# Kernel tuning notes

Hardware: AMD Instinct MI355X
Metric: run time of the kernel (lower is better)

## Reference

```python
import jax, jax.numpy as jnp
import numpy as np

B, S, D, H, FF = 4, 2048, 1024, 16, 4096
HD = D // H
EPS = 1e-5


def layer_norm(x, g, b):
    mu = jnp.mean(x, axis=-1, keepdims=True)
    var = jnp.mean(jnp.square(x - mu), axis=-1, keepdims=True)
    return (x - mu) * jax.lax.rsqrt(var + EPS) * g + b


def setup_inputs() -> dict:
    key = jax.random.key(0)
    ks = jax.random.split(key, 8)
    s_d = 1.0 / np.sqrt(D)
    s_ff = 1.0 / np.sqrt(FF)
    return {
        "x": jax.random.normal(ks[0], (B, S, D), dtype=jnp.float32),
        "Wq": jax.random.normal(ks[1], (D, D), dtype=jnp.float32) * s_d,
        "bq": jnp.zeros((D,), jnp.float32),
        "Wk": jax.random.normal(ks[2], (D, D), dtype=jnp.float32) * s_d,
        "bk": jnp.zeros((D,), jnp.float32),
        "Wv": jax.random.normal(ks[3], (D, D), dtype=jnp.float32) * s_d,
        "bv": jnp.zeros((D,), jnp.float32),
        "g1": jnp.ones((D,), jnp.float32),
        "beta1": jnp.zeros((D,), jnp.float32),
        "g2": jnp.ones((D,), jnp.float32),
        "beta2": jnp.zeros((D,), jnp.float32),
        "W1": jax.random.normal(ks[4], (D, FF), dtype=jnp.float32) * s_d,
        "b1": jnp.zeros((FF,), jnp.float32),
        "W2": jax.random.normal(ks[5], (FF, D), dtype=jnp.float32) * s_ff,
        "b2": jnp.zeros((D,), jnp.float32),
    }


def reference(x, Wq, bq, Wk, bk, Wv, bv, g1, beta1, g2, beta2, W1, b1, W2, b2):
    # pre-LN attention (self.layer_norm in the original)
    h = layer_norm(x, g1, beta1)
    q = (h @ Wq + bq).reshape(B, S, H, HD)
    k = (h @ Wk + bk).reshape(B, S, H, HD)
    v = (h @ Wv + bv).reshape(B, S, H, HD)
    scores = jnp.einsum("bqhd,bkhd->bhqk", q, k) / np.sqrt(HD)
    probs = jax.nn.softmax(scores, axis=-1)
    attn = jnp.einsum("bhqk,bkhd->bqhd", probs, v).reshape(B, S, D)
    y = attn + x
    # second LN (self.LN), then FFN; note original adds residual from LN output
    f = layer_norm(y, g2, beta2)
    ff = jnp.maximum(f @ W1 + b1, 0.0) @ W2 + b2
    return f + ff
```

## Files before the change

### kernel.cpp

```cpp
#include <hip/hip_runtime.h>
#include <hip/hip_bf16.h>
#include <cstdint>
#include <cstddef>

#define B_   4
#define S_   2048
#define D_   1024
#define H_   16
#define HD_  64
#define FF_  4096
#define MTOT (B_*S_)

typedef __bf16 bf16;
typedef bf16  bf16x8 __attribute__((ext_vector_type(8)));
typedef bf16  bf16x4 __attribute__((ext_vector_type(4)));
typedef float f32x4  __attribute__((ext_vector_type(4)));

#define LOG2E 1.44269504088896340736f

__device__ __forceinline__ void async16(const bf16* g, bf16* l) {
  __builtin_amdgcn_global_load_lds(
      (const __attribute__((address_space(1))) unsigned int*)g,
      (__attribute__((address_space(3))) unsigned int*)l,
      16, 0, 0);
}

__global__ void wcast_t(const float* __restrict__ W, bf16* __restrict__ Wt,
                        int K, int N) {
  __shared__ float t[32][33];
  const int k0 = blockIdx.y * 32, n0 = blockIdx.x * 32;
  const int tx = threadIdx.x, ty = threadIdx.y;
#pragma unroll
  for (int r = ty; r < 32; r += 8)
    t[r][tx] = W[(size_t)(k0 + r) * N + n0 + tx];
  __syncthreads();
#pragma unroll
  for (int r = ty; r < 32; r += 8)
    Wt[(size_t)(n0 + r) * K + k0 + tx] = (bf16)t[tx][r];
}

__global__ void ln_fused(const float* __restrict__ xin, const float* __restrict__ res,
                         const float* __restrict__ gamma, const float* __restrict__ beta,
                         bf16* __restrict__ out) {
  const int row = blockIdx.x, tid = threadIdx.x;
  const int lane = tid & 63, w = tid >> 6;
  f32x4 v = *(const f32x4*)(xin + (size_t)row * D_ + tid * 4);
  if (res) {
    f32x4 r = *(const f32x4*)(res + (size_t)row * D_ + tid * 4);
    v += r;
  }
  float sum = v[0] + v[1] + v[2] + v[3];
  float sq  = v[0]*v[0] + v[1]*v[1] + v[2]*v[2] + v[3]*v[3];
#pragma unroll
  for (int d = 1; d < 64; d <<= 1) {
    sum += __shfl_xor(sum, d);
    sq  += __shfl_xor(sq, d);
  }
  __shared__ float red[8];
  if (lane == 0) { red[w] = sum; red[4 + w] = sq; }
  __syncthreads();
  sum = red[0] + red[1] + red[2] + red[3];
  sq  = red[4] + red[5] + red[6] + red[7];
  const float mu   = sum * (1.f / D_);
  const float rstd = rsqrtf(sq * (1.f / D_) - mu * mu + 1e-5f);
  f32x4 g  = *(const f32x4*)(gamma + tid * 4);
  f32x4 bt = *(const f32x4*)(beta  + tid * 4);
  bf16x4 ov;
#pragma unroll
  for (int j = 0; j < 4; j++)
    ov[j] = (bf16)((v[j] - mu) * rstd * g[j] + bt[j]);
  *(bf16x4*)(out + (size_t)row * D_ + tid * 4) = ov;
}

template <int EPI>
__global__ void gemm_bt(const bf16* __restrict__ A, const bf16* __restrict__ Bt,
                        const float* __restrict__ bias, void* __restrict__ Cout,
                        const bf16* __restrict__ addf, int M, int N, int K) {
  __shared__ bf16 As[128 * 32];
  __shared__ bf16 Bs[128 * 32];
  const int tid = threadIdx.x;
  const int lane = tid & 63;
  const int w = tid >> 6;
  const int wm = w >> 1, wn = w & 1;
  const int bm = blockIdx.y * 128;
  const int bn = blockIdx.x * 128;
  const int rg = lane >> 4, rl = lane & 15;

  const bf16* ga = A  + (size_t)(bm + w * 16 + (lane >> 2)) * K + (lane & 3) * 8;
  const bf16* gb = Bt + (size_t)(bn + w * 16 + (lane >> 2)) * K + (lane & 3) * 8;
  bf16* la = As + w * 512;
  bf16* lb = Bs + w * 512;
  const size_t rowadv = (size_t)64 * K;

  f32x4 acc[4][4];
  const f32x4 z = {0.f, 0.f, 0.f, 0.f};
#pragma unroll
  for (int m = 0; m < 4; m++)
#pragma unroll
    for (int n = 0; n < 4; n++) acc[m][n] = z;

  for (int kt = 0; kt < K; kt += 32) {
    __syncthreads();
    async16(ga,          la);
    async16(ga + rowadv, la + 2048);
    async16(gb,          lb);
    async16(gb + rowadv, lb + 2048);
    ga += 32; gb += 32;
    __syncthreads();

    bf16x8 af[4], bfr[4];
#pragma unroll
    for (int m = 0; m < 4; m++)
      af[m] = *(const bf16x8*)(As + (wm * 64 + m * 16 + rl) * 32 + rg * 8);
#pragma unroll
    for (int n = 0; n < 4; n++)
      bfr[n] = *(const bf16x8*)(Bs + (wn * 64 + n * 16 + rl) * 32 + rg * 8);
#pragma unroll
    for (int m = 0; m < 4; m++)
#pragma unroll
      for (int n = 0; n < 4; n++)
        acc[m][n] = __builtin_amdgcn_mfma_f32_16x16x32_bf16(af[m], bfr[n], acc[m][n], 0, 0, 0);
  }

#pragma unroll
  for (int m = 0; m < 4; m++) {
    const int row0 = bm + wm * 64 + m * 16 + rg * 4;
#pragma unroll
    for (int n = 0; n < 4; n++) {
      const int col = bn + wn * 64 + n * 16 + rl;
      const float bb = bias[col];
#pragma unroll
      for (int i = 0; i < 4; i++) {
        const int row = row0 + i;
        float v = acc[m][n][i] + bb;
        if (EPI == 3) {
          ((bf16*)Cout)[(size_t)row * N + col] = (bf16)fmaxf(v, 0.f);
        } else {
          ((float*)Cout)[(size_t)row * N + col] =
              v + (float)addf[(size_t)row * N + col];
        }
      }
    }
  }
}

__global__ void gemm_qkv(const bf16* __restrict__ A, const bf16* __restrict__ Bt,
                         const float* __restrict__ bq, const float* __restrict__ bk,
                         const float* __restrict__ bv, bf16* __restrict__ qout,
                         bf16* __restrict__ kout, bf16* __restrict__ vtout) {
  const int K = 1024;
  __shared__ bf16 As[128 * 32];
  __shared__ bf16 Bs[128 * 32];
  const int tid = threadIdx.x;
  const int lane = tid & 63;
  const int w = tid >> 6;
  const int wm = w >> 1, wn = w & 1;
  const int bm = blockIdx.y * 128;
  const int bn = blockIdx.x * 128;
  const int rg = lane >> 4, rl = lane & 15;

  const bf16* ga = A  + (size_t)(bm + w * 16 + (lane >> 2)) * K + (lane & 3) * 8;
  const bf16* gb = Bt + (size_t)(bn + w * 16 + (lane >> 2)) * K + (lane & 3) * 8;
  bf16* la = As + w * 512;
  bf16* lb = Bs + w * 512;
  const size_t rowadv = (size_t)64 * K;

  f32x4 acc[4][4];
  const f32x4 z = {0.f, 0.f, 0.f, 0.f};
#pragma unroll
  for (int m = 0; m < 4; m++)
#pragma unroll
    for (int n = 0; n < 4; n++) acc[m][n] = z;

  for (int kt = 0; kt < K; kt += 32) {
    __syncthreads();
    async16(ga,          la);
    async16(ga + rowadv, la + 2048);
    async16(gb,          lb);
    async16(gb + rowadv, lb + 2048);
    ga += 32; gb += 32;
    __syncthreads();

    bf16x8 af[4], bfr[4];
#pragma unroll
    for (int m = 0; m < 4; m++)
      af[m] = *(const bf16x8*)(As + (wm * 64 + m * 16 + rl) * 32 + rg * 8);
#pragma unroll
    for (int n = 0; n < 4; n++)
      bfr[n] = *(const bf16x8*)(Bs + (wn * 64 + n * 16 + rl) * 32 + rg * 8);
#pragma unroll
    for (int m = 0; m < 4; m++)
#pragma unroll
      for (int n = 0; n < 4; n++)
        acc[m][n] = __builtin_amdgcn_mfma_f32_16x16x32_bf16(af[m], bfr[n], acc[m][n], 0, 0, 0);
  }

  const int sector = bn >> 10;
#pragma unroll
  for (int m = 0; m < 4; m++) {
    const int row0 = bm + wm * 64 + m * 16 + rg * 4;
#pragma unroll
    for (int n = 0; n < 4; n++) {
      const int col = bn + wn * 64 + n * 16 + rl;
      const int cl = col & 1023;
      const float bb = (sector == 0) ? bq[cl] : (sector == 1 ? bk[cl] : bv[cl]);
#pragma unroll
      for (int i = 0; i < 4; i++) {
        const int row = row0 + i;
        const float v = acc[m][n][i] + bb;
        if (sector == 0) {
          qout[(size_t)row * D_ + cl] = (bf16)(v * (0.125f * LOG2E));
        } else if (sector == 1) {
          kout[(size_t)row * D_ + cl] = (bf16)v;
        } else {
          const int b = row >> 11, s = row & 2047;
          const int h = cl >> 6, hd = cl & 63;
          vtout[(((size_t)(b * H_ + h) * HD_ + hd) << 11) + s] = (bf16)v;
        }
      }
    }
  }
}

__global__ __launch_bounds__(512, 4)
void attn_fwd(const bf16* __restrict__ Q, const bf16* __restrict__ Kb,
              const bf16* __restrict__ Vt, float* __restrict__ O) {
  __shared__ bf16 Ks[2][64 * 64];
  __shared__ bf16 Vs[2][64 * 64];
  __shared__ bf16 Pl[8][32][72];
  const int tid = threadIdx.x, lane = tid & 63, w = tid >> 6;
  const int rg = lane >> 4, rl = lane & 15;
  const int bh = blockIdx.y, b = bh >> 4, h = bh & 15;
  const int q0 = blockIdx.x * 256 + w * 32;

  const bf16* qp = Q + ((size_t)b * S_ + q0) * D_ + h * HD_;
  const bf16* kp = Kb + (size_t)b * S_ * D_ + h * HD_;
  const bf16* vp = Vt + (size_t)bh * HD_ * S_;

  const int sr = lane >> 3;
  const int sc = (lane & 7) ^ sr;

#define STAGE(buf, t)                                                          \
  {                                                                            \
    const int row = w * 8 + sr;                                                \
    async16(kp + (size_t)((t) * 64 + row) * D_ + sc * 8, &Ks[buf][w * 8 * 64]);\
    async16(vp + (size_t)row * S_ + (t) * 64 + sc * 8,  &Vs[buf][w * 8 * 64]); \
  }

  bf16x8 qf[2][2];
#pragma unroll
  for (int m = 0; m < 2; m++)
#pragma unroll
    for (int kc = 0; kc < 2; kc++)
      qf[m][kc] = *(const bf16x8*)(qp + (size_t)(m * 16 + rl) * D_ + kc * 32 + rg * 8);

  const f32x4 z = {0.f, 0.f, 0.f, 0.f};
  f32x4 o[2][4];
  float mr[2], lr[2];
#pragma unroll
  for (int m = 0; m < 2; m++) {
    mr[m] = -1e30f; lr[m] = 0.f;
#pragma unroll
    for (int np = 0; np < 4; np++) o[m][np] = z;
  }

  STAGE(0, 0);
  __syncthreads();

  int cur = 0;
  for (int t = 0; t < S_ / 64; ++t) {
    if (t + 1 < S_ / 64) STAGE(cur ^ 1, t + 1);
    const bf16* Kc = Ks[cur];
    const bf16* Vc = Vs[cur];

    bf16x8 kf[4][2];
#pragma unroll
    for (int n = 0; n < 4; n++) {
      const int krow = n * 16 + rl;
#pragma unroll
      for (int kc = 0; kc < 2; kc++)
        kf[n][kc] = *(const bf16x8*)(Kc + krow * 64 + (((kc * 4 + rg) ^ (krow & 7)) * 8));
    }

    f32x4 s[2][4];
#pragma unroll
    for (int m = 0; m < 2; m++)
#pragma unroll
      for (int n = 0; n < 4; n++) s[m][n] = z;
#pragma unroll
    for (int kc = 0; kc < 2; kc++)
#pragma unroll
      for (int n = 0; n < 4; n++)
#pragma unroll
        for (int m = 0; m < 2; m++)
          s[m][n] = __builtin_amdgcn_mfma_f32_16x16x32_bf16(kf[n][kc], qf[m][kc], s[m][n], 0, 0, 0);

#pragma unroll
    for (int m = 0; m < 2; m++) {
      float x0 = fmaxf(fmaxf(s[m][0][0], s[m][0][1]), fmaxf(s[m][0][2], s[m][0][3]));
      float x1 = fmaxf(fmaxf(s[m][1][0], s[m][1][1]), fmaxf(s[m][1][2], s[m][1][3]));
      float x2 = fmaxf(fmaxf(s[m][2][0], s[m][2][1]), fmaxf(s[m][2][2], s[m][2][3]));
      float x3 = fmaxf(fmaxf(s[m][3][0], s[m][3][1]), fmaxf(s[m][3][2], s[m][3][3]));
      float vmax = fmaxf(fmaxf(x0, x1), fmaxf(x2, x3));
      vmax = fmaxf(vmax, __shfl_xor(vmax, 16));
      vmax = fmaxf(vmax, __shfl_xor(vmax, 32));
      const float mnew = fmaxf(mr[m], vmax);
      const float corr = __builtin_amdgcn_exp2f(mr[m] - mnew);
      mr[m] = mnew;
      float ps = 0.f;
#pragma unroll
      for (int n = 0; n < 4; n++)
#pragma unroll
        for (int i = 0; i < 4; i++) {
          const float p = __builtin_amdgcn_exp2f(s[m][n][i] - mnew);
          s[m][n][i] = p;
          ps += p;
        }
      ps += __shfl_xor(ps, 16);
      ps += __shfl_xor(ps, 32);
      lr[m] = lr[m] * corr + ps;
#pragma unroll
      for (int np = 0; np < 4; np++)
#pragma unroll
        for (int i = 0; i < 4; i++) o[m][np][i] *= corr;
#pragma unroll
      for (int n = 0; n < 4; n++) {
        bf16x4 pv;
#pragma unroll
        for (int i = 0; i < 4; i++) pv[i] = (bf16)s[m][n][i];
        *(bf16x4*)&Pl[w][m * 16 + rl][n * 16 + rg * 4] = pv;
      }
    }

    bf16x8 pf[2][2];
#pragma unroll
    for (int m = 0; m < 2; m++)
#pragma unroll
      for (int kc = 0; kc < 2; kc++)
        pf[m][kc] = *(const bf16x8*)&Pl[w][m * 16 + rl][kc * 32 + rg * 8];

    bf16x8 vf[4][2];
#pragma unroll
    for (int np = 0; np < 4; np++) {
      const int vrow = np * 16 + rl;
#pragma unroll
      for (int kc = 0; kc < 2; kc++)
        vf[np][kc] = *(const bf16x8*)(Vc + vrow * 64 + (((kc * 4 + rg) ^ (vrow & 7)) * 8));
    }

#pragma unroll
    for (int kc = 0; kc < 2; kc++)
#pragma unroll
      for (int np = 0; np < 4; np++)
#pragma unroll
        for (int m = 0; m < 2; m++)
          o[m][np] = __builtin_amdgcn_mfma_f32_16x16x32_bf16(vf[np][kc], pf[m][kc], o[m][np], 0, 0, 0);

    __syncthreads();
    cur ^= 1;
  }
#undef STAGE

#pragma unroll
  for (int m = 0; m < 2; m++) {
    const float inv = 1.f / lr[m];
    const size_t rowb = ((size_t)b * S_ + q0 + m * 16 + rl) * D_ + h * HD_;
#pragma unroll
    for (int np = 0; np < 4; np++) {
      f32x4 ov;
#pragma unroll
      for (int i = 0; i < 4; i++) ov[i] = o[m][np][i] * inv;
      *(f32x4*)(O + rowb + np * 16 + rg * 4) = ov;
    }
  }
}

extern "C" void kernel_launch(void* const* d_in, const int* in_sizes, int n_in,
                              void* d_out, int out_size, void* d_ws, size_t ws_size,
                              hipStream_t stream) {
  (void)in_sizes; (void)n_in; (void)out_size; (void)ws_size;
  const float* x   = (const float*)d_in[0];
  const float* Wq  = (const float*)d_in[1];
  const float* bq  = (const float*)d_in[2];
  const float* Wk  = (const float*)d_in[3];
  const float* bk  = (const float*)d_in[4];
  const float* Wv  = (const float*)d_in[5];
  const float* bv  = (const float*)d_in[6];
  const float* g1  = (const float*)d_in[7];
  const float* be1 = (const float*)d_in[8];
  const float* g2  = (const float*)d_in[9];
  const float* be2 = (const float*)d_in[10];
  const float* W1  = (const float*)d_in[11];
  const float* b1  = (const float*)d_in[12];
  const float* W2  = (const float*)d_in[13];
  const float* b2  = (const float*)d_in[14];
  float* out = (float*)d_out;

  char* p = (char*)d_ws;
  const size_t MB = (size_t)1 << 20;
  bf16*  wqkv = (bf16*)(p + 0 * MB);
  bf16*  w1t  = (bf16*)(p + 6 * MB);
  bf16*  w2t  = (bf16*)(p + 14 * MB);
  bf16*  hb   = (bf16*)(p + 22 * MB);
  bf16*  qb   = (bf16*)(p + 38 * MB);
  bf16*  kb   = (bf16*)(p + 54 * MB);
  bf16*  vt   = (bf16*)(p + 70 * MB);
  float* at   = (float*)(p + 86 * MB);
  bf16*  fb   = (bf16*)(p + 118 * MB);
  bf16*  ff1  = (bf16*)(p + 22 * MB);

  const dim3 tb(32, 8);
  wcast_t<<<dim3(32, 32),  tb, 0, stream>>>(Wq, wqkv,                1024, 1024);
  wcast_t<<<dim3(32, 32),  tb, 0, stream>>>(Wk, wqkv + 1024 * 1024,  1024, 1024);
  wcast_t<<<dim3(32, 32),  tb, 0, stream>>>(Wv, wqkv + 2048 * 1024,  1024, 1024);
  wcast_t<<<dim3(128, 32), tb, 0, stream>>>(W1, w1t, 1024, 4096);
  wcast_t<<<dim3(32, 128), tb, 0, stream>>>(W2, w2t, 4096, 1024);

  ln_fused<<<MTOT, 256, 0, stream>>>(x, nullptr, g1, be1, hb);

  gemm_qkv<<<dim3(24, 64), 256, 0, stream>>>(hb, wqkv, bq, bk, bv, qb, kb, vt);

  attn_fwd<<<dim3(8, 64), 512, 0, stream>>>(qb, kb, vt, at);

  ln_fused<<<MTOT, 256, 0, stream>>>(at, x, g2, be2, fb);

  gemm_bt<3><<<dim3(32, 64), 256, 0, stream>>>(fb, w1t, b1, ff1, nullptr, MTOT, 4096, 1024);
  gemm_bt<4><<<dim3(8, 64),  256, 0, stream>>>(ff1, w2t, b2, out, fb, MTOT, 1024, 4096);
}
```

Before: 544.8 us.

## Replace GEMMs with 256x256 double-buffered swizzled-LDS tiles and grouped block order

Replaces the 128x128, single-buffered GEMM kernels (QKV, FFN1, FFN2) with one templated 256x256 tile kernel that uses 512 threads and a K-step of 64. Global-to-LDS async loads are double-buffered, so the next tile loads while the current one computes, and the LDS rows use an XOR swizzle to avoid bank conflicts. Blocks are launched on a 1D grid with a grouped swizzle for L2 reuse. The cost is 128KB of LDS per block, which means low occupancy, and far fewer blocks (128 for FFN2 on 256 CUs), which risks underfilling the GPU.

```diff
diff --git a/kernel.cpp b/kernel.cpp
--- a/kernel.cpp
+++ b/kernel.cpp
@@ -73,149 +73,136 @@
 }
 
 template <int EPI>
-__global__ void gemm_bt(const bf16* __restrict__ A, const bf16* __restrict__ Bt,
-                        const float* __restrict__ bias, void* __restrict__ Cout,
-                        const bf16* __restrict__ addf, int M, int N, int K) {
-  __shared__ bf16 As[128 * 32];
-  __shared__ bf16 Bs[128 * 32];
+__global__ __launch_bounds__(512)
+void gemm256(const bf16* __restrict__ A, const bf16* __restrict__ Bt,
+             const float* __restrict__ bias, void* __restrict__ Cout,
+             const bf16* __restrict__ addf,
+             const float* __restrict__ bq, const float* __restrict__ bk,
+             const float* __restrict__ bv, bf16* __restrict__ qout,
+             bf16* __restrict__ kout, bf16* __restrict__ vtout,
+             int M, int N, int K) {
+  __shared__ bf16 As[2][256 * 64];
+  __shared__ bf16 Bs[2][256 * 64];
   const int tid = threadIdx.x;
   const int lane = tid & 63;
   const int w = tid >> 6;
-  const int wm = w >> 1, wn = w & 1;
-  const int bm = blockIdx.y * 128;
-  const int bn = blockIdx.x * 128;
+  const int wm = w >> 2, wn = w & 3;
   const int rg = lane >> 4, rl = lane & 15;
-
-  const bf16* ga = A  + (size_t)(bm + w * 16 + (lane >> 2)) * K + (lane & 3) * 8;
-  const bf16* gb = Bt + (size_t)(bn + w * 16 + (lane >> 2)) * K + (lane & 3) * 8;
-  bf16* la = As + w * 512;
-  bf16* lb = Bs + w * 512;
-  const size_t rowadv = (size_t)64 * K;
-
-  f32x4 acc[4][4];
+  const int sr = lane >> 3;
+  const int sc = (lane & 7) ^ sr;
+
+  const int nbn = N >> 8;
+  const int cpx = (int)gridDim.x >> 3;
+  const int bid = (int)blockIdx.x;
+  const int swz = (bid & 7) * cpx + (bid >> 3);
+  const int bm = (swz / nbn) << 8;
+  const int bn = (swz % nbn) << 8;
+
+  const bf16* gA0 = A  + (size_t)(bm + w * 8 + sr) * K + sc * 8;
+  const bf16* gB0 = Bt + (size_t)(bn + w * 8 + sr) * K + sc * 8;
+  const size_t i64K = (size_t)64 * K;
+
+#define GSTAGE(slot, t)                                                        \
+  {                                                                            \
+    const bf16* ga_ = gA0 + (size_t)(t) * 64;                                  \
+    const bf16* gb_ = gB0 + (size_t)(t) * 64;                                  \
+    _Pragma("unroll")                                                          \
+    for (int i_ = 0; i_ < 4; i_++) {                                           \
+      async16(ga_ + i_ * i64K, &As[slot][(i_ * 64 + w * 8) * 64]);             \
+      async16(gb_ + i_ * i64K, &Bs[slot][(i_ * 64 + w * 8) * 64]);             \
+    }                                                                          \
+  }
+
+#define COMPUTE(slotbuf)                                                       \
+  {                                                                            \
+    const bf16* Ac = &As[slotbuf][0];                                          \
+    const bf16* Bc = &Bs[slotbuf][0];                                          \
+    _Pragma("unroll")                                                          \
+    for (int kk = 0; kk < 2; kk++) {                                           \
+      bf16x8 af[8], bw[4];                                                     \
+      _Pragma("unroll")                                                        \
+      for (int mi = 0; mi < 8; mi++)                                           \
+        af[mi] = *(const bf16x8*)(Ac + (wm * 128 + mi * 16 + rl) * 64 +        \
+                                  (((kk * 4 + rg) ^ (rl & 7)) * 8));           \
+      _Pragma("unroll")                                                        \
+      for (int ni = 0; ni < 4; ni++)                                           \
+        bw[ni] = *(const bf16x8*)(Bc + (wn * 64 + ni * 16 + rl) * 64 +         \
+                                  (((kk * 4 + rg) ^ (rl & 7)) * 8));           \
+      _Pragma("unroll")                                                        \
+      for (int mi = 0; mi < 8; mi++)                                           \
+        _Pragma("unroll")                                                      \
+        for (int ni = 0; ni < 4; ni++)                                         \
+          acc[mi][ni] = __builtin_amdgcn_mfma_f32_16x16x32_bf16(               \
+              af[mi], bw[ni], acc[mi][ni], 0, 0, 0);                           \
+    }                                                                          \
+  }
+
+  f32x4 acc[8][4];
   const f32x4 z = {0.f, 0.f, 0.f, 0.f};
 #pragma unroll
-  for (int m = 0; m < 4; m++)
-#pragma unroll
-    for (int n = 0; n < 4; n++) acc[m][n] = z;
-
-  for (int kt = 0; kt < K; kt += 32) {
-    __syncthreads();
-    async16(ga,          la);
-    async16(ga + rowadv, la + 2048);
-    async16(gb,          lb);
-    async16(gb + rowadv, lb + 2048);
-    ga += 32; gb += 32;
-    __syncthreads();
-
-    bf16x8 af[4], bfr[4];
-#pragma unroll
-    for (int m = 0; m < 4; m++)
-      af[m] = *(const bf16x8*)(As + (wm * 64 + m * 16 + rl) * 32 + rg * 8);
-#pragma unroll
-    for (int n = 0; n < 4; n++)
-      bfr[n] = *(const bf16x8*)(Bs + (wn * 64 + n * 16 + rl) * 32 + rg * 8);
-#pragma unroll
-    for (int m = 0; m < 4; m++)
-#pragma unroll
-      for (int n = 0; n < 4; n++)
-        acc[m][n] = __builtin_amdgcn_mfma_f32_16x16x32_bf16(af[m], bfr[n], acc[m][n], 0, 0, 0);
-  }
-
-#pragma unroll
-  for (int m = 0; m < 4; m++) {
-    const int row0 = bm + wm * 64 + m * 16 + rg * 4;
-#pragma unroll
-    for (int n = 0; n < 4; n++) {
-      const int col = bn + wn * 64 + n * 16 + rl;
-      const float bb = bias[col];
-#pragma unroll
-      for (int i = 0; i < 4; i++) {
-        const int row = row0 + i;
-        float v = acc[m][n][i] + bb;
-        if (EPI == 3) {
-          ((bf16*)Cout)[(size_t)row * N + col] = (bf16)fmaxf(v, 0.f);
-        } else {
-          ((float*)Cout)[(size_t)row * N + col] =
-              v + (float)addf[(size_t)row * N + col];
-        }
-      }
-    }
-  }
-}
-
-__global__ void gemm_qkv(const bf16* __restrict__ A, const bf16* __restrict__ Bt,
-                         const float* __restrict__ bq, const float* __restrict__ bk,
-                         const float* __restrict__ bv, bf16* __restrict__ qout,
-                         bf16* __restrict__ kout, bf16* __restrict__ vtout) {
-  const int K = 1024;
-  __shared__ bf16 As[128 * 32];
-  __shared__ bf16 Bs[128 * 32];
-  const int tid = threadIdx.x;
-  const int lane = tid & 63;
-  const int w = tid >> 6;
-  const int wm = w >> 1, wn = w & 1;
-  const int bm = blockIdx.y * 128;
-  const int bn = blockIdx.x * 128;
-  const int rg = lane >> 4, rl = lane & 15;
-
-  const bf16* ga = A  + (size_t)(bm + w * 16 + (lane >> 2)) * K + (lane & 3) * 8;
-  const bf16* gb = Bt + (size_t)(bn + w * 16 + (lane >> 2)) * K + (lane & 3) * 8;
-  bf16* la = As + w * 512;
-  bf16* lb = Bs + w * 512;
-  const size_t rowadv = (size_t)64 * K;
-
-  f32x4 acc[4][4];
-  const f32x4 z = {0.f, 0.f, 0.f, 0.f};
-#pragma unroll
-  for (int m = 0; m < 4; m++)
-#pragma unroll
-    for (int n = 0; n < 4; n++) acc[m][n] = z;
-
-  for (int kt = 0; kt < K; kt += 32) {
-    __syncthreads();
-    async16(ga,          la);
-    async16(ga + rowadv, la + 2048);
-    async16(gb,          lb);
-    async16(gb + rowadv, lb + 2048);
-    ga += 32; gb += 32;
-    __syncthreads();
-
-    bf16x8 af[4], bfr[4];
-#pragma unroll
-    for (int m = 0; m < 4; m++)
-      af[m] = *(const bf16x8*)(As + (wm * 64 + m * 16 + rl) * 32 + rg * 8);
-#pragma unroll
-    for (int n = 0; n < 4; n++)
-      bfr[n] = *(const bf16x8*)(Bs + (wn * 64 + n * 16 + rl) * 32 + rg * 8);
-#pragma unroll
-    for (int m = 0; m < 4; m++)
-#pragma unroll
-      for (int n = 0; n < 4; n++)
-        acc[m][n] = __builtin_amdgcn_mfma_f32_16x16x32_bf16(af[m], bfr[n], acc[m][n], 0, 0, 0);
-  }
-
-  const int sector = bn >> 10;
-#pragma unroll
-  for (int m = 0; m < 4; m++) {
-    const int row0 = bm + wm * 64 + m * 16 + rg * 4;
-#pragma unroll
-    for (int n = 0; n < 4; n++) {
-      const int col = bn + wn * 64 + n * 16 + rl;
-      const int cl = col & 1023;
-      const float bb = (sector == 0) ? bq[cl] : (sector == 1 ? bk[cl] : bv[cl]);
-#pragma unroll
-      for (int i = 0; i < 4; i++) {
-        const int row = row0 + i;
-        const float v = acc[m][n][i] + bb;
-        if (sector == 0) {
-          qout[(size_t)row * D_ + cl] = (bf16)(v * (0.125f * LOG2E));
-        } else if (sector == 1) {
-          kout[(size_t)row * D_ + cl] = (bf16)v;
-        } else {
-          const int b = row >> 11, s = row & 2047;
-          const int h = cl >> 6, hd = cl & 63;
-          vtout[(((size_t)(b * H_ + h) * HD_ + hd) << 11) + s] = (bf16)v;
+  for (int mi = 0; mi < 8; mi++)
+#pragma unroll
+    for (int ni = 0; ni < 4; ni++) acc[mi][ni] = z;
+
+  const int NT = K >> 6;
+  GSTAGE(0, 0);
+  GSTAGE(1, 1);
+
+  for (int t = 0; t < NT - 1; ++t) {
+    asm volatile("s_waitcnt vmcnt(8)" ::: "memory");
+    __builtin_amdgcn_sched_barrier(0);
+    __builtin_amdgcn_s_barrier();
+    __builtin_amdgcn_sched_barrier(0);
+    COMPUTE(t & 1);
+    __builtin_amdgcn_sched_barrier(0);
+    __builtin_amdgcn_s_barrier();
+    __builtin_amdgcn_sched_barrier(0);
+    if (t + 2 < NT) GSTAGE(t & 1, t + 2);
+  }
+  asm volatile("s_waitcnt vmcnt(0)" ::: "memory");
+  __builtin_amdgcn_sched_barrier(0);
+  __builtin_amdgcn_s_barrier();
+  __builtin_amdgcn_sched_barrier(0);
+  COMPUTE((NT - 1) & 1);
+
+#undef GSTAGE
+#undef COMPUTE
+
+#pragma unroll
+  for (int mi = 0; mi < 8; mi++) {
+    const int row0 = bm + wm * 128 + mi * 16 + rg * 4;
+#pragma unroll
+    for (int ni = 0; ni < 4; ni++) {
+      const int col = bn + wn * 64 + ni * 16 + rl;
+      if (EPI == 3) {
+        const float bb = bias[col];
+#pragma unroll
+        for (int i = 0; i < 4; i++)
+          ((bf16*)Cout)[(size_t)(row0 + i) * N + col] =
+              (bf16)fmaxf(acc[mi][ni][i] + bb, 0.f);
+      } else if (EPI == 4) {
+        const float bb = bias[col];
+#pragma unroll
+        for (int i = 0; i < 4; i++)
+          ((float*)Cout)[(size_t)(row0 + i) * N + col] =
+              acc[mi][ni][i] + bb + (float)addf[(size_t)(row0 + i) * N + col];
+      } else {
+        const int sector = bn >> 10;
+        const int cl = col & 1023;
+        const float bb = (sector == 0) ? bq[cl] : (sector == 1 ? bk[cl] : bv[cl]);
+#pragma unroll
+        for (int i = 0; i < 4; i++) {
+          const int row = row0 + i;
+          const float v = acc[mi][ni][i] + bb;
+          if (sector == 0) {
+            qout[(size_t)row * D_ + cl] = (bf16)(v * (0.125f * LOG2E));
+          } else if (sector == 1) {
+            kout[(size_t)row * D_ + cl] = (bf16)v;
+          } else {
+            const int b = row >> 11, s = row & 2047;
+            const int h = cl >> 6, hd = cl & 63;
+            vtout[(((size_t)(b * H_ + h) * HD_ + hd) << 11) + s] = (bf16)v;
+          }
         }
       }
     }
@@ -418,12 +405,17 @@
 
   ln_fused<<<MTOT, 256, 0, stream>>>(x, nullptr, g1, be1, hb);
 
-  gemm_qkv<<<dim3(24, 64), 256, 0, stream>>>(hb, wqkv, bq, bk, bv, qb, kb, vt);
+  gemm256<5><<<384, 512, 0, stream>>>(hb, wqkv, nullptr, nullptr, nullptr,
+                                      bq, bk, bv, qb, kb, vt, MTOT, 3072, 1024);
 
   attn_fwd<<<dim3(8, 64), 512, 0, stream>>>(qb, kb, vt, at);
 
   ln_fused<<<MTOT, 256, 0, stream>>>(at, x, g2, be2, fb);
 
-  gemm_bt<3><<<dim3(32, 64), 256, 0, stream>>>(fb, w1t, b1, ff1, nullptr, MTOT, 4096, 1024);
-  gemm_bt<4><<<dim3(8, 64),  256, 0, stream>>>(ff1, w2t, b2, out, fb, MTOT, 1024, 4096);
-}
+  gemm256<3><<<512, 512, 0, stream>>>(fb, w1t, b1, ff1, nullptr,
+                                      nullptr, nullptr, nullptr, nullptr, nullptr, nullptr,
+                                      MTOT, 4096, 1024);
+  gemm256<4><<<128, 512, 0, stream>>>(ff1, w2t, b2, out, fb,
+                                      nullptr, nullptr, nullptr, nullptr, nullptr, nullptr,
+                                      MTOT, 1024, 4096);
+}
```

Measured after the change: 575.8 us. 1.06x slower.
